# Kernel optimization log

Hardware: AMD Instinct MI355X
Metric: run time of the kernel (lower is better)

Reference implementation:

```python
import jax, jax.numpy as jnp
import numpy as np

DECAY = 0.99
EPS = 1e-05
COMMIT = 0.25


def setup_inputs() -> dict:
    key = jax.random.key(0)
    k1, k2 = jax.random.split(key)
    dim, n_embed = 256, 8192
    z = jax.random.normal(k1, (32, 32, 32, dim), dtype=jnp.float32)
    embed = jax.random.normal(k2, (dim, n_embed), dtype=jnp.float32)
    cluster_size = jnp.zeros((n_embed,), dtype=jnp.float32)
    embed_avg = embed  # torch init: embed_avg = embed.clone()
    return {"z": z, "embed": embed, "cluster_size": cluster_size, "embed_avg": embed_avg}


def reference(z, embed, cluster_size, embed_avg):
    dim, n_embed = embed.shape
    flatten = z.reshape(-1, dim)                       # [N, D]
    # squared L2 distance to each code: ||f||^2 - 2 f.E + ||E||^2
    dist = ((flatten ** 2).sum(1, keepdims=True)
            - 2.0 * flatten @ embed
            + (embed ** 2).sum(0, keepdims=True))      # [N, K]
    ind = jnp.argmin(dist, axis=1)                     # [N]
    quantize = jnp.take(embed.T, ind, axis=0).reshape(z.shape)
    embed_ind = ind.reshape(z.shape[:-1])

    # EMA codebook update (training mode), via segment_sum instead of a dense one-hot
    counts = jax.ops.segment_sum(jnp.ones_like(ind, dtype=flatten.dtype), ind,
                                 num_segments=n_embed)          # [K]
    embed_sum = jax.ops.segment_sum(flatten, ind,
                                    num_segments=n_embed).T     # [D, K]
    cluster_size_new = cluster_size * DECAY + (1.0 - DECAY) * counts
    embed_avg_new = embed_avg * DECAY + (1.0 - DECAY) * embed_sum
    n = cluster_size_new.sum()
    cs = (cluster_size_new + EPS) / (n + n_embed * EPS) * n
    embed_new = embed_avg_new / cs[None, :]

    diff = COMMIT * jnp.mean((jax.lax.stop_gradient(quantize) - z) ** 2)
    quantize_st = z + jax.lax.stop_gradient(quantize - z)  # straight-through
    return quantize_st, diff, embed_ind, embed_new
```

## Files before the change

### kernel.cpp

```cpp
#include <hip/hip_runtime.h>
#include <hip/hip_bf16.h>

#define D 256
#define K 8192
#define NTOT 32768
#define BM 128
#define BN2 128
#define CSPLIT 4
#define CT_PER (K / CSPLIT / BN2)

typedef __bf16 bf16x8 __attribute__((ext_vector_type(8)));
typedef float f32x4 __attribute__((ext_vector_type(4)));

__device__ __forceinline__ void gl_lds16(const void* g, void* l) {
    __builtin_amdgcn_global_load_lds(
        (__attribute__((address_space(1))) void*)(g),
        (__attribute__((address_space(3))) void*)(l), 16, 0, 0);
}

__device__ __forceinline__ unsigned int enc_f32(float f) {
    unsigned int u = __float_as_uint(f);
    return (u & 0x80000000u) ? ~u : (u | 0x80000000u);
}

__device__ __forceinline__ unsigned short f2bfu(float x) {
    __hip_bfloat16 h = __float2bfloat16(x);
    return __builtin_bit_cast(unsigned short, h);
}
__device__ __forceinline__ float bfu2f(unsigned short u) {
    return __bfloat162float(__builtin_bit_cast(__hip_bfloat16, u));
}

__global__ __launch_bounds__(256)
void conv_F(const float* __restrict__ z, unsigned short* __restrict__ Fhi,
            unsigned short* __restrict__ Flo) {
    int i4 = blockIdx.x * 256 + threadIdx.x;
    float4 v = ((const float4*)z)[i4];
    ushort4 h, l;
    h.x = f2bfu(v.x); l.x = f2bfu(v.x - bfu2f(h.x));
    h.y = f2bfu(v.y); l.y = f2bfu(v.y - bfu2f(h.y));
    h.z = f2bfu(v.z); l.z = f2bfu(v.z - bfu2f(h.z));
    h.w = f2bfu(v.w); l.w = f2bfu(v.w - bfu2f(h.w));
    ((ushort4*)Fhi)[i4] = h;
    ((ushort4*)Flo)[i4] = l;
}

__global__ __launch_bounds__(256)
void conv_E(const float* __restrict__ E, unsigned short* __restrict__ EhiT,
            unsigned short* __restrict__ EloT, float* __restrict__ ET) {
    __shared__ float tile[64][65];
    int tid = threadIdx.x;
    int k0 = blockIdx.x * 64, d0 = blockIdx.y * 64;
#pragma unroll
    for (int it = 0; it < 16; ++it) {
        int idx = it * 256 + tid;
        int dr = idx >> 6, kc = idx & 63;
        tile[kc][dr] = E[(d0 + dr) * K + k0 + kc];
    }
    __syncthreads();
#pragma unroll
    for (int it = 0; it < 16; ++it) {
        int idx = it * 256 + tid;
        int kr = idx >> 6, dc = idx & 63;
        float v = tile[kr][dc];
        unsigned short h = f2bfu(v);
        int o = (k0 + kr) * D + d0 + dc;
        EhiT[o] = h;
        EloT[o] = f2bfu(v - bfu2f(h));
        ET[o] = v;
    }
}

__global__ __launch_bounds__(256)
void enorm_kernel(const float* __restrict__ E, float* __restrict__ enorm) {
    int k = blockIdx.x * 256 + threadIdx.x;
    float s = 0.f;
    for (int d = 0; d < D; ++d) {
        float v = E[d * K + k];
        s += v * v;
    }
    enorm[k] = s;
}

__global__ __launch_bounds__(256)
void mfma_dist_argmin(const unsigned short* __restrict__ Fhi,
                      const unsigned short* __restrict__ Flo,
                      const unsigned short* __restrict__ EhiT,
                      const unsigned short* __restrict__ EloT,
                      const float* __restrict__ enorm,
                      unsigned long long* __restrict__ bestpack) {
    __shared__ unsigned short lds[2][4][BM * 32];

    const int tid = threadIdx.x;
    const int wave = tid >> 6;
    const int lane = tid & 63;
    const int qd = lane >> 4;
    const int ln = lane & 15;
    const int wm = (wave >> 1) * 64;
    const int wn = (wave & 1) * 64;
    const int n0 = blockIdx.x * BM;
    const int c0 = blockIdx.y * (K / CSPLIT);

    const int r_ = tid >> 2;
    const int s_sw = (tid & 3) ^ ((tid >> 3) & 3);

    const int csw = (qd ^ ((ln >> 1) & 3)) * 8;
    int aro[4], bro[4];
#pragma unroll
    for (int mi = 0; mi < 4; ++mi) aro[mi] = (wm + mi * 16 + ln) * 32 + csw;
#pragma unroll
    for (int ni = 0; ni < 4; ++ni) bro[ni] = (wn + ni * 16 + ln) * 32 + csw;

    float bestv[16];
    int besti[16];
#pragma unroll
    for (int i = 0; i < 16; ++i) { bestv[i] = 3.402823466e38f; besti[i] = 0; }

    auto load_stage = [&](int buf, int ct, int d0) {
        const int cb0 = c0 + ct * BN2;
#pragma unroll
        for (int it = 0; it < 2; ++it) {
            const int ga = (n0 + it * 64 + r_) * D + d0 + s_sw * 8;
            const int gb = (cb0 + it * 64 + r_) * D + d0 + s_sw * 8;
            const int lo = it * 2048 + wave * 512;
            gl_lds16(Fhi + ga, &lds[buf][0][lo]);
            gl_lds16(Flo + ga, &lds[buf][1][lo]);
            gl_lds16(EhiT + gb, &lds[buf][2][lo]);
            gl_lds16(EloT + gb, &lds[buf][3][lo]);
        }
    };

    load_stage(0, 0, 0);

    for (int ct = 0; ct < CT_PER; ++ct) {
        const int cb = c0 + ct * BN2;
        float en[4];
#pragma unroll
        for (int ni = 0; ni < 4; ++ni) en[ni] = enorm[cb + wn + ni * 16 + ln];

        f32x4 acc[4][4];
#pragma unroll
        for (int mi = 0; mi < 4; ++mi)
#pragma unroll
            for (int ni = 0; ni < 4; ++ni) acc[mi][ni] = (f32x4){0.f, 0.f, 0.f, 0.f};

#pragma unroll
        for (int dd = 0; dd < 8; ++dd) {
            const int b = (ct * 8 + dd) & 1;
            __syncthreads();
            int nct = ct, ndd = dd + 1;
            if (ndd == 8) { ndd = 0; nct = ct + 1; }
            if (nct < CT_PER) load_stage(b ^ 1, nct, ndd * 32);

            bf16x8 ah[4], al[4], bh[4], bl[4];
#pragma unroll
            for (int mi = 0; mi < 4; ++mi) {
                ah[mi] = *(const bf16x8*)&lds[b][0][aro[mi]];
                al[mi] = *(const bf16x8*)&lds[b][1][aro[mi]];
            }
#pragma unroll
            for (int ni = 0; ni < 4; ++ni) {
                bh[ni] = *(const bf16x8*)&lds[b][2][bro[ni]];
                bl[ni] = *(const bf16x8*)&lds[b][3][bro[ni]];
            }
#pragma unroll
            for (int mi = 0; mi < 4; ++mi)
#pragma unroll
                for (int ni = 0; ni < 4; ++ni)
                    acc[mi][ni] = __builtin_amdgcn_mfma_f32_16x16x32_bf16(
                        ah[mi], bh[ni], acc[mi][ni], 0, 0, 0);
#pragma unroll
            for (int mi = 0; mi < 4; ++mi)
#pragma unroll
                for (int ni = 0; ni < 4; ++ni)
                    acc[mi][ni] = __builtin_amdgcn_mfma_f32_16x16x32_bf16(
                        ah[mi], bl[ni], acc[mi][ni], 0, 0, 0);
#pragma unroll
            for (int mi = 0; mi < 4; ++mi)
#pragma unroll
                for (int ni = 0; ni < 4; ++ni)
                    acc[mi][ni] = __builtin_amdgcn_mfma_f32_16x16x32_bf16(
                        al[mi], bh[ni], acc[mi][ni], 0, 0, 0);
        }

#pragma unroll
        for (int ni = 0; ni < 4; ++ni) {
            int k = cb + wn + ni * 16 + ln;
#pragma unroll
            for (int mi = 0; mi < 4; ++mi) {
                f32x4 a = acc[mi][ni];
#pragma unroll
                for (int r = 0; r < 4; ++r) {
                    float dist = en[ni] - 2.0f * a[r];
                    int bi = mi * 4 + r;
                    if (dist < bestv[bi]) { bestv[bi] = dist; besti[bi] = k; }
                }
            }
        }
    }

#pragma unroll
    for (int mi = 0; mi < 4; ++mi) {
#pragma unroll
        for (int r = 0; r < 4; ++r) {
            int bi = mi * 4 + r;
            float v = bestv[bi];
            int ix = besti[bi];
#pragma unroll
            for (int off = 1; off < 16; off <<= 1) {
                float v2 = __shfl_xor(v, off);
                int i2 = __shfl_xor(ix, off);
                if (v2 < v || (v2 == v && i2 < ix)) { v = v2; ix = i2; }
            }
            if (ln == 0) {
                int m = n0 + wm + mi * 16 + qd * 4 + r;
                unsigned long long pack =
                    ((unsigned long long)enc_f32(v) << 32) | (unsigned int)ix;
                atomicMin(&bestpack[m], pack);
            }
        }
    }
}

#define ROWS_PER_BLOCK 64
__global__ __launch_bounds__(256)
void assign_apply(const float* __restrict__ z,
                  const float* __restrict__ ET,
                  const unsigned long long* __restrict__ bestpack,
                  float* __restrict__ out_q, float* __restrict__ out_ind,
                  float* __restrict__ out_diff,
                  float* __restrict__ counts, float* __restrict__ esumT) {
    const int tx = threadIdx.x;
    const int rbase = blockIdx.x * ROWS_PER_BLOCK;
    float part = 0.f;
    for (int r = 0; r < ROWS_PER_BLOCK; ++r) {
        int n = rbase + r;
        unsigned long long p = bestpack[n];
        int idx = (int)(p & 0xFFFFFFFFull);
        float f = z[n * D + tx];
        float q = ET[idx * D + tx];
        out_q[n * D + tx] = q;
        float dd = q - f;
        part += dd * dd;
        atomicAdd(&esumT[idx * D + tx], f);
        if (tx == 0) {
            atomicAdd(&counts[idx], 1.0f);
            out_ind[n] = (float)idx;
        }
    }
#pragma unroll
    for (int off = 32; off; off >>= 1) part += __shfl_down(part, off);
    __shared__ float wsum[4];
    if ((tx & 63) == 0) wsum[tx >> 6] = part;
    __syncthreads();
    if (tx == 0) {
        float t = wsum[0] + wsum[1] + wsum[2] + wsum[3];
        atomicAdd(out_diff, t * (0.25f / 8388608.0f));
    }
}

__global__ __launch_bounds__(1024)
void csn_sum(const float* __restrict__ cs_in, const float* __restrict__ counts,
             float* __restrict__ csn, float* __restrict__ nsum) {
    const float decay = 0.99f;
    const float omd = 0.01f;
    int tx = threadIdx.x;
    float p = 0.f;
    for (int k = tx; k < K; k += 1024) {
        float v = decay * cs_in[k] + omd * counts[k];
        csn[k] = v;
        p += v;
    }
#pragma unroll
    for (int off = 32; off; off >>= 1) p += __shfl_down(p, off);
    __shared__ float red[16];
    if ((tx & 63) == 0) red[tx >> 6] = p;
    __syncthreads();
    if (tx == 0) {
        float t = 0.f;
        for (int i = 0; i < 16; ++i) t += red[i];
        nsum[0] = t;
    }
}

__global__ __launch_bounds__(256)
void finalize(const float* __restrict__ eavg, const float* __restrict__ esumT,
              const float* __restrict__ csn, const float* __restrict__ nsum,
              float* __restrict__ out_enew) {
    const float decay = 0.99f;
    const float omd = 0.01f;
    const float keps = (float)(8192 * 1e-5);
    int idx = blockIdx.x * 256 + threadIdx.x;
    float nv = nsum[0];
    int k = idx & (K - 1);
    int d = idx >> 13;
    float avg_new = decay * eavg[idx] + omd * esumT[k * D + d];
    float cs = (csn[k] + 1e-5f) / (nv + keps) * nv;
    out_enew[idx] = avg_new / cs;
}

extern "C" void kernel_launch(void* const* d_in, const int* in_sizes, int n_in,
                              void* d_out, int out_size, void* d_ws, size_t ws_size,
                              hipStream_t stream) {
    const float* z = (const float*)d_in[0];
    const float* embed = (const float*)d_in[1];
    const float* cs_in = (const float*)d_in[2];
    const float* eavg = (const float*)d_in[3];

    float* out = (float*)d_out;
    float* out_q = out;
    float* out_diff = out + 8388608;
    float* out_ind = out + 8388609;
    float* out_enew = out + 8421377;

    char* ws = (char*)d_ws;
    unsigned long long* bestpack = (unsigned long long*)ws;
    float* enorm = (float*)(ws + 262144);
    float* counts = (float*)(ws + 294912);
    float* csn = (float*)(ws + 327680);
    float* nsum = (float*)(ws + 360448);
    float* esumT = (float*)(ws + 360704);
    unsigned short* Fhi = (unsigned short*)(ws + 8749312);
    unsigned short* Flo = (unsigned short*)(ws + 25526528);
    unsigned short* EhiT = (unsigned short*)(ws + 42303744);
    unsigned short* EloT = (unsigned short*)(ws + 46498048);
    float* ET = (float*)(ws + 50692352);

    hipMemsetAsync(bestpack, 0xFF, NTOT * 8, stream);
    hipMemsetAsync(counts, 0, K * 4, stream);
    hipMemsetAsync(esumT, 0, K * D * 4, stream);
    hipMemsetAsync(out_diff, 0, 4, stream);

    conv_F<<<NTOT * D / 4 / 256, 256, 0, stream>>>(z, Fhi, Flo);
    conv_E<<<dim3(K / 64, D / 64), 256, 0, stream>>>(embed, EhiT, EloT, ET);
    enorm_kernel<<<K / 256, 256, 0, stream>>>(embed, enorm);
    mfma_dist_argmin<<<dim3(NTOT / BM, CSPLIT), 256, 0, stream>>>(Fhi, Flo, EhiT, EloT,
                                                                  enorm, bestpack);
    assign_apply<<<NTOT / ROWS_PER_BLOCK, 256, 0, stream>>>(z, ET, bestpack, out_q,
                                                            out_ind, out_diff, counts, esumT);
    csn_sum<<<1, 1024, 0, stream>>>(cs_in, counts, csn, nsum);
    finalize<<<(D * K) / 256, 256, 0, stream>>>(eavg, esumT, csn, nsum, out_enew);
}
```

Baseline: 654.3 us.

## Split hi/lo bf16 stages into alternating half-buffers to halve LDS footprint

Replaces the double-buffered stage that held hi and lo parts of both operands with two single buffers: one for the hi parts and one for the lo parts. The lo loads overlap the hi MFMA pass, and the next hi loads overlap the lo MFMA passes. This halves shared memory and reduces live fragment registers, which could raise occupancy. In exchange it adds a second barrier per K-step and shorter overlap windows for each load.

```diff
diff --git a/kernel.cpp b/kernel.cpp
--- a/kernel.cpp
+++ b/kernel.cpp
@@ -89,7 +89,7 @@
                       const unsigned short* __restrict__ EloT,
                       const float* __restrict__ enorm,
                       unsigned long long* __restrict__ bestpack) {
-    __shared__ unsigned short lds[2][4][BM * 32];
+    __shared__ unsigned short lds[2][2][BM * 32];
 
     const int tid = threadIdx.x;
     const int wave = tid >> 6;
@@ -116,21 +116,21 @@
 #pragma unroll
     for (int i = 0; i < 16; ++i) { bestv[i] = 3.402823466e38f; besti[i] = 0; }
 
-    auto load_stage = [&](int buf, int ct, int d0) {
+    auto load_half = [&](int buf, int ct, int d0, int lo) {
         const int cb0 = c0 + ct * BN2;
+        const unsigned short* SA = lo ? Flo : Fhi;
+        const unsigned short* SB = lo ? EloT : EhiT;
 #pragma unroll
         for (int it = 0; it < 2; ++it) {
             const int ga = (n0 + it * 64 + r_) * D + d0 + s_sw * 8;
             const int gb = (cb0 + it * 64 + r_) * D + d0 + s_sw * 8;
-            const int lo = it * 2048 + wave * 512;
-            gl_lds16(Fhi + ga, &lds[buf][0][lo]);
-            gl_lds16(Flo + ga, &lds[buf][1][lo]);
-            gl_lds16(EhiT + gb, &lds[buf][2][lo]);
-            gl_lds16(EloT + gb, &lds[buf][3][lo]);
+            const int lo_off = it * 2048 + wave * 512;
+            gl_lds16(SA + ga, &lds[buf][0][lo_off]);
+            gl_lds16(SB + gb, &lds[buf][1][lo_off]);
         }
     };
 
-    load_stage(0, 0, 0);
+    load_half(0, 0, 0, 0);
 
     for (int ct = 0; ct < CT_PER; ++ct) {
         const int cb = c0 + ct * BN2;
@@ -146,29 +146,32 @@
 
 #pragma unroll
         for (int dd = 0; dd < 8; ++dd) {
-            const int b = (ct * 8 + dd) & 1;
+            const int d0 = dd * 32;
+            __syncthreads();
+            load_half(1, ct, d0, 1);
+
+            bf16x8 ah[4], bh[4];
+#pragma unroll
+            for (int mi = 0; mi < 4; ++mi) ah[mi] = *(const bf16x8*)&lds[0][0][aro[mi]];
+#pragma unroll
+            for (int ni = 0; ni < 4; ++ni) bh[ni] = *(const bf16x8*)&lds[0][1][bro[ni]];
+#pragma unroll
+            for (int mi = 0; mi < 4; ++mi)
+#pragma unroll
+                for (int ni = 0; ni < 4; ++ni)
+                    acc[mi][ni] = __builtin_amdgcn_mfma_f32_16x16x32_bf16(
+                        ah[mi], bh[ni], acc[mi][ni], 0, 0, 0);
+
             __syncthreads();
             int nct = ct, ndd = dd + 1;
             if (ndd == 8) { ndd = 0; nct = ct + 1; }
-            if (nct < CT_PER) load_stage(b ^ 1, nct, ndd * 32);
-
-            bf16x8 ah[4], al[4], bh[4], bl[4];
-#pragma unroll
-            for (int mi = 0; mi < 4; ++mi) {
-                ah[mi] = *(const bf16x8*)&lds[b][0][aro[mi]];
-                al[mi] = *(const bf16x8*)&lds[b][1][aro[mi]];
-            }
-#pragma unroll
-            for (int ni = 0; ni < 4; ++ni) {
-                bh[ni] = *(const bf16x8*)&lds[b][2][bro[ni]];
-                bl[ni] = *(const bf16x8*)&lds[b][3][bro[ni]];
-            }
-#pragma unroll
-            for (int mi = 0; mi < 4; ++mi)
-#pragma unroll
-                for (int ni = 0; ni < 4; ++ni)
-                    acc[mi][ni] = __builtin_amdgcn_mfma_f32_16x16x32_bf16(
-                        ah[mi], bh[ni], acc[mi][ni], 0, 0, 0);
+            if (nct < CT_PER) load_half(0, nct, ndd * 32, 0);
+
+            bf16x8 al[4], bl[4];
+#pragma unroll
+            for (int mi = 0; mi < 4; ++mi) al[mi] = *(const bf16x8*)&lds[1][0][aro[mi]];
+#pragma unroll
+            for (int ni = 0; ni < 4; ++ni) bl[ni] = *(const bf16x8*)&lds[1][1][bro[ni]];
 #pragma unroll
             for (int mi = 0; mi < 4; ++mi)
 #pragma unroll
```

Result: slower. 691.5 us (+5.7%).
